# Kernel optimization log

Measured on AMD Instinct MI355X. Metric: run time of the kernel, lower is better.

Reference implementation:

```python
import jax, jax.numpy as jnp
import numpy as np

B, N, D = 2, 2048, 2048
H, HKV, HD = 16, 4, 128  # n_heads, n_kv_heads, head_dim
G = H // HKV             # GQA group size


def setup_inputs() -> dict:
    key = jax.random.key(0)
    ks = jax.random.split(key, 5)
    x = jax.random.normal(ks[0], (B, N, D), jnp.float32)
    # rotary angles: standard 10000-base frequencies, half head_dim
    inv_freq = 1.0 / (10000.0 ** (jnp.arange(HD // 2, dtype=jnp.float32) / (HD // 2)))
    ang = jnp.arange(N, dtype=jnp.float32)[:, None] * inv_freq[None, :]  # [N, HD/2]
    cos = jnp.cos(ang)[None, :, None, :]  # [1, N, 1, HD/2]
    sin = jnp.sin(ang)[None, :, None, :]
    attn_mask = jnp.ones((B, N), jnp.float32)
    s = 0.02
    Wq = jax.random.normal(ks[1], (D, H * HD), jnp.float32) * s
    Wkv = jax.random.normal(ks[2], (D, 2 * HKV * HD), jnp.float32) * s
    Wo = jax.random.normal(ks[3], (H * HD, D), jnp.float32) * s
    bo = jnp.zeros((D,), jnp.float32)
    return {"x": x, "cos": cos, "sin": sin, "attn_mask": attn_mask,
            "Wq": Wq, "Wkv": Wkv, "Wo": Wo, "bo": bo}


def _rope(t, cos, sin):
    # t: [b, n, h, d]; rotate-half style split at d//2
    d2 = t.shape[-1] // 2
    t1, t2 = t[..., :d2], t[..., d2:]
    return jnp.concatenate([t1 * cos + t2 * sin, t2 * cos - t1 * sin], axis=-1)


def reference(x, cos, sin, attn_mask, Wq, Wkv, Wo, bo):
    b, n, _ = x.shape
    q = (x @ Wq).reshape(b, n, H, HD)
    kv = x @ Wkv
    k, v = jnp.split(kv, 2, axis=-1)
    k = k.reshape(b, n, HKV, HD)
    v = v.reshape(b, n, HKV, HD)
    q = _rope(q, cos, sin)
    k = _rope(k, cos, sin)
    # b n h d -> b h n d; group q heads: head H_idx maps to kv head H_idx % HKV
    # (einops '(r h)' repeat pattern => q reshaped as [b, G, HKV, n, d])
    q = q.transpose(0, 2, 1, 3).reshape(b, G, HKV, n, HD)
    k = k.transpose(0, 2, 1, 3)  # [b, HKV, n, d]
    v = v.transpose(0, 2, 1, 3)
    scale = HD ** -0.5
    attn = jnp.einsum('bghnd,bhmd->bghnm', q, k) * scale
    bias = (1.0 - attn_mask) * -1e9  # [b, n_keys]
    attn = attn + bias[:, None, None, None, :]
    attn = jax.nn.softmax(attn, axis=-1)
    out = jnp.einsum('bghnm,bhmd->bghnd', attn, v)
    # b (g h) n d -> b n (g h d)
    out = out.transpose(0, 3, 1, 2, 4).reshape(b, n, H * HD)
    return out @ Wo + bo
```

## Files before the change

### kernel.cpp

```cpp
#include <hip/hip_runtime.h>
#include <hip/hip_bf16.h>
#include <cstddef>

#define NB    2
#define NSEQ  2048
#define DMODEL 2048
#define NH    16
#define NKV   4
#define HDIM  128

typedef __attribute__((ext_vector_type(8))) short short8;
typedef __attribute__((ext_vector_type(4))) short short4v;
typedef __attribute__((ext_vector_type(4))) float floatx4;
typedef const __attribute__((address_space(1))) void* gptr_t;
typedef __attribute__((address_space(3))) void* lptr_t;

#if __has_builtin(__builtin_amdgcn_exp2f)
#define EXP2F(x) __builtin_amdgcn_exp2f(x)
#else
#define EXP2F(x) __expf((x) * 0.6931471805599453f)
#endif

__device__ inline unsigned short f2bf(float f) {
    unsigned int u = __float_as_uint(f);
    u += 0x7fffu + ((u >> 16) & 1u);
    return (unsigned short)(u >> 16);
}

__device__ inline floatx4 fzero4() {
    floatx4 v; v[0] = 0.f; v[1] = 0.f; v[2] = 0.f; v[3] = 0.f; return v;
}

__global__ void cast_f32_bf16(const float* __restrict__ in,
                              unsigned short* __restrict__ out, int n4) {
    int i = blockIdx.x * blockDim.x + threadIdx.x;
    if (i >= n4) return;
    float4 v = ((const float4*)in)[i];
    ushort4 o;
    o.x = f2bf(v.x); o.y = f2bf(v.y); o.z = f2bf(v.z); o.w = f2bf(v.w);
    ((ushort4*)out)[i] = o;
}

__global__ void transpose_cast(const float* __restrict__ W,
                               unsigned short* __restrict__ Wt, int K, int N) {
    __shared__ float tile[32][33];
    int tx = threadIdx.x, ty = threadIdx.y;
    int n0 = blockIdx.x * 32, k0 = blockIdx.y * 32;
#pragma unroll
    for (int i = 0; i < 4; i++)
        tile[ty + i * 8][tx] = W[(size_t)(k0 + ty + i * 8) * N + n0 + tx];
    __syncthreads();
#pragma unroll
    for (int i = 0; i < 4; i++)
        Wt[(size_t)(n0 + ty + i * 8) * K + k0 + tx] = f2bf(tile[tx][ty + i * 8]);
}

__global__ __launch_bounds__(256, 2) void gemm_bt(
    const unsigned short* __restrict__ A,
    const unsigned short* __restrict__ Bt,
    float* __restrict__ C,
    const float* __restrict__ bias,
    int M, int N, int K) {
    __shared__ __align__(16) unsigned short As[128 * 32];
    __shared__ __align__(16) unsigned short Bs[128 * 32];
    const int t = threadIdx.x;
    const int m0 = blockIdx.y * 128, n0 = blockIdx.x * 128;
    const int lane = t & 63, wave = t >> 6;
    const int ln = lane & 15, quad = lane >> 4;
    const int wm = (wave >> 1) * 64, wn = (wave & 1) * 64;
    floatx4 acc[4][4];
#pragma unroll
    for (int r = 0; r < 4; r++)
#pragma unroll
        for (int c = 0; c < 4; c++) acc[r][c] = fzero4();

    const int r0 = t >> 2, c0 = (t & 3) * 8;
    const int r1 = (t + 256) >> 2, c1 = ((t + 256) & 3) * 8;

    for (int kt = 0; kt < K; kt += 32) {
        const unsigned short* ga0 = A + (size_t)(m0 + r0) * K + kt + c0;
        const unsigned short* ga1 = A + (size_t)(m0 + r1) * K + kt + c1;
        const unsigned short* gb0 = Bt + (size_t)(n0 + r0) * K + kt + c0;
        const unsigned short* gb1 = Bt + (size_t)(n0 + r1) * K + kt + c1;
        __builtin_amdgcn_global_load_lds((gptr_t)ga0, (lptr_t)(As + t * 8), 16, 0, 0);
        __builtin_amdgcn_global_load_lds((gptr_t)ga1, (lptr_t)(As + (t + 256) * 8), 16, 0, 0);
        __builtin_amdgcn_global_load_lds((gptr_t)gb0, (lptr_t)(Bs + t * 8), 16, 0, 0);
        __builtin_amdgcn_global_load_lds((gptr_t)gb1, (lptr_t)(Bs + (t + 256) * 8), 16, 0, 0);
        __syncthreads();
        short8 af[4], bfr[4];
#pragma unroll
        for (int r = 0; r < 4; r++)
            af[r] = *(const short8*)(As + (wm + r * 16 + ln) * 32 + quad * 8);
#pragma unroll
        for (int c = 0; c < 4; c++)
            bfr[c] = *(const short8*)(Bs + (wn + c * 16 + ln) * 32 + quad * 8);
#pragma unroll
        for (int r = 0; r < 4; r++)
#pragma unroll
            for (int c = 0; c < 4; c++)
                acc[r][c] = __builtin_amdgcn_mfma_f32_16x16x32_bf16(af[r], bfr[c], acc[r][c], 0, 0, 0);
        __syncthreads();
    }
#pragma unroll
    for (int r = 0; r < 4; r++) {
        int mb = m0 + wm + r * 16 + quad * 4;
#pragma unroll
        for (int c = 0; c < 4; c++) {
            int col = n0 + wn + c * 16 + ln;
            float bv = bias ? bias[col] : 0.f;
#pragma unroll
            for (int g = 0; g < 4; g++)
                C[(size_t)(mb + g) * N + col] = acc[r][c][g] + bv;
        }
    }
}

__global__ __launch_bounds__(256, 2) void gemm_qkv_rope(
    const unsigned short* __restrict__ A,
    const unsigned short* __restrict__ Bt,
    const float* __restrict__ cosb,
    const float* __restrict__ sinb,
    unsigned short* __restrict__ Qb,
    unsigned short* __restrict__ Kb,
    unsigned short* __restrict__ Vt) {
    const int K = DMODEL;
    __shared__ __align__(16) unsigned short As[128 * 32];
    __shared__ __align__(16) unsigned short Bs[128 * 32];
    __shared__ __align__(16) unsigned short Vx[128 * 136];
    const int t = threadIdx.x;
    const int m0 = blockIdx.y * 128, n0 = blockIdx.x * 128;
    const int lane = t & 63, wave = t >> 6;
    const int ln = lane & 15, quad = lane >> 4;
    const int wm = (wave >> 1) * 64, bq = (wave & 1) * 32;
    floatx4 acc[4][4];
#pragma unroll
    for (int r = 0; r < 4; r++)
#pragma unroll
        for (int c = 0; c < 4; c++) acc[r][c] = fzero4();

    const int r0 = t >> 2, c0 = (t & 3) * 8;
    const int r1 = (t + 256) >> 2, c1 = ((t + 256) & 3) * 8;

    for (int kt = 0; kt < K; kt += 32) {
        const unsigned short* ga0 = A + (size_t)(m0 + r0) * K + kt + c0;
        const unsigned short* ga1 = A + (size_t)(m0 + r1) * K + kt + c1;
        const unsigned short* gb0 = Bt + (size_t)(n0 + r0) * K + kt + c0;
        const unsigned short* gb1 = Bt + (size_t)(n0 + r1) * K + kt + c1;
        __builtin_amdgcn_global_load_lds((gptr_t)ga0, (lptr_t)(As + t * 8), 16, 0, 0);
        __builtin_amdgcn_global_load_lds((gptr_t)ga1, (lptr_t)(As + (t + 256) * 8), 16, 0, 0);
        __builtin_amdgcn_global_load_lds((gptr_t)gb0, (lptr_t)(Bs + t * 8), 16, 0, 0);
        __builtin_amdgcn_global_load_lds((gptr_t)gb1, (lptr_t)(Bs + (t + 256) * 8), 16, 0, 0);
        __syncthreads();
        short8 af[4], bfr[4];
#pragma unroll
        for (int r = 0; r < 4; r++)
            af[r] = *(const short8*)(As + (wm + r * 16 + ln) * 32 + quad * 8);
#pragma unroll
        for (int c = 0; c < 4; c++)
            bfr[c] = *(const short8*)(
                Bs + (bq + (c & 1) * 16 + (c >> 1) * 64 + ln) * 32 + quad * 8);
#pragma unroll
        for (int r = 0; r < 4; r++)
#pragma unroll
            for (int c = 0; c < 4; c++)
                acc[r][c] = __builtin_amdgcn_mfma_f32_16x16x32_bf16(af[r], bfr[c], acc[r][c], 0, 0, 0);
        __syncthreads();
    }

    if (n0 < 2048) {
        const float qs = (float)(0.08838834764831845 * 1.4426950408889634);
        int h = n0 >> 7;
#pragma unroll
        for (int r = 0; r < 4; r++)
#pragma unroll
            for (int c = 0; c < 2; c++)
#pragma unroll
                for (int g = 0; g < 4; g++) {
                    int row = m0 + wm + r * 16 + quad * 4 + g;
                    int b = row >> 11, n = row & 2047;
                    int j = bq + c * 16 + ln;
                    float cv = cosb[n * 64 + j], sv = sinb[n * 64 + j];
                    float t1 = acc[r][c][g], t2 = acc[r][c + 2][g];
                    unsigned short* qp = Qb + ((size_t)(b * NH + h) * NSEQ + n) * 128;
                    qp[j]      = f2bf((t1 * cv + t2 * sv) * qs);
                    qp[j + 64] = f2bf((t2 * cv - t1 * sv) * qs);
                }
    } else if (n0 < 2560) {
        int hk = (n0 - 2048) >> 7;
#pragma unroll
        for (int r = 0; r < 4; r++)
#pragma unroll
            for (int c = 0; c < 2; c++)
#pragma unroll
                for (int g = 0; g < 4; g++) {
                    int row = m0 + wm + r * 16 + quad * 4 + g;
                    int b = row >> 11, n = row & 2047;
                    int j = bq + c * 16 + ln;
                    float cv = cosb[n * 64 + j], sv = sinb[n * 64 + j];
                    float t1 = acc[r][c][g], t2 = acc[r][c + 2][g];
                    unsigned short* kp = Kb + ((size_t)(b * NKV + hk) * NSEQ + n) * 128;
                    kp[j]      = f2bf(t1 * cv + t2 * sv);
                    kp[j + 64] = f2bf(t2 * cv - t1 * sv);
                }
    } else {
        int hk = (n0 - 2560) >> 7;
#pragma unroll
        for (int r = 0; r < 4; r++)
#pragma unroll
            for (int c = 0; c < 4; c++) {
                int d = bq + (c & 1) * 16 + (c >> 1) * 64 + ln;
                int s = wm + (r >> 1) * 32 + quad * 8 + (r & 1) * 4;
#pragma unroll
                for (int g = 0; g < 4; g++)
                    Vx[d * 136 + s + g] = f2bf(acc[r][c][g]);
            }
        __syncthreads();
        int b = m0 >> 11, nloc = m0 & 2047;
#pragma unroll
        for (int pass = 0; pass < 2; pass++) {
            int d = pass * 64 + (t >> 2), q4 = t & 3;
            unsigned short* vp =
                Vt + ((size_t)(b * NKV + hk) * 128 + d) * NSEQ + nloc + q4 * 32;
#pragma unroll
            for (int i = 0; i < 4; i++)
                *(short8*)(vp + i * 8) = *(const short8*)(Vx + d * 136 + q4 * 32 + i * 8);
        }
    }
}

__global__ __launch_bounds__(256, 2) void attn_k(
    const unsigned short* __restrict__ Qb,
    const unsigned short* __restrict__ Kb,
    const unsigned short* __restrict__ Vt,
    const float* __restrict__ mask,
    unsigned short* __restrict__ Ab) {
    __shared__ __align__(16) unsigned short Ks[2 * 64 * 128];
    __shared__ __align__(16) unsigned short Vs[2 * 128 * 64];
    const int t = threadIdx.x, wave = t >> 6, lane = t & 63;
    const int ln = lane & 15, quad = lane >> 4;
    const int y = blockIdx.y, b = y >> 4, h = y & 15, kv = h & 3;
    const int q0 = blockIdx.x * 128;

    const unsigned short* Kbase = Kb + (size_t)(b * NKV + kv) * NSEQ * 128;
    const unsigned short* Vbase = Vt + (size_t)(b * NKV + kv) * 128 * NSEQ;
    const float* mbase = mask + b * NSEQ;

    const unsigned short* Qp =
        Qb + ((size_t)(b * NH + h) * NSEQ + q0 + wave * 32 + ln) * 128;
    short8 qf[2][4];
#pragma unroll
    for (int rt = 0; rt < 2; rt++)
#pragma unroll
        for (int kc = 0; kc < 4; kc++)
            qf[rt][kc] = *(const short8*)(Qp + rt * 16 * 128 + kc * 32 + quad * 8);

    floatx4 Oacc[2][8];
#pragma unroll
    for (int rt = 0; rt < 2; rt++)
#pragma unroll
        for (int d = 0; d < 8; d++) Oacc[rt][d] = fzero4();
    floatx4 Lacc[2];
    Lacc[0] = fzero4(); Lacc[1] = fzero4();

    short8 ones8;
#pragma unroll
    for (int i = 0; i < 8; i++) ones8[i] = (short)0x3F80;

    {
#pragma unroll
        for (int i = 0; i < 4; i++) {
            int c = i * 256 + t, r = c >> 4, c8 = c & 15;
            __builtin_amdgcn_global_load_lds(
                (gptr_t)(Kbase + (size_t)r * 128 + ((c8 ^ (r & 7)) * 8)),
                (lptr_t)(Ks + c * 8), 16, 0, 0);
        }
#pragma unroll
        for (int i = 0; i < 4; i++) {
            int c = i * 256 + t, dr = c >> 3, c8 = c & 7;
            __builtin_amdgcn_global_load_lds(
                (gptr_t)(Vbase + (size_t)dr * NSEQ + ((c8 ^ (dr & 7)) * 8)),
                (lptr_t)(Vs + c * 8), 16, 0, 0);
        }
    }
    __syncthreads();

    for (int it = 0; it < NSEQ / 64; ++it) {
        const int kt = it * 64, cb = it & 1;
        const int ktn = (kt + 64) & (NSEQ - 1);
        unsigned short* Kn = Ks + (cb ^ 1) * 8192;
        unsigned short* Vn = Vs + (cb ^ 1) * 8192;
#pragma unroll
        for (int i = 0; i < 4; i++) {
            int c = i * 256 + t, r = c >> 4, c8 = c & 15;
            __builtin_amdgcn_global_load_lds(
                (gptr_t)(Kbase + (size_t)(ktn + r) * 128 + ((c8 ^ (r & 7)) * 8)),
                (lptr_t)(Kn + c * 8), 16, 0, 0);
        }
#pragma unroll
        for (int i = 0; i < 4; i++) {
            int c = i * 256 + t, dr = c >> 3, c8 = c & 7;
            __builtin_amdgcn_global_load_lds(
                (gptr_t)(Vbase + (size_t)dr * NSEQ + ktn + ((c8 ^ (dr & 7)) * 8)),
                (lptr_t)(Vn + c * 8), 16, 0, 0);
        }

        floatx4 biasv[4];
#pragma unroll
        for (int nj = 0; nj < 4; nj++) {
            float4 mb = *(const float4*)(mbase + kt + nj * 16 + quad * 4);
            biasv[nj][0] = (1.f - mb.x) * -1.4426950408889634e9f;
            biasv[nj][1] = (1.f - mb.y) * -1.4426950408889634e9f;
            biasv[nj][2] = (1.f - mb.z) * -1.4426950408889634e9f;
            biasv[nj][3] = (1.f - mb.w) * -1.4426950408889634e9f;
        }

        const unsigned short* Kc = Ks + cb * 8192;
        const unsigned short* Vc = Vs + cb * 8192;

        floatx4 sacc[2][4];
#pragma unroll
        for (int rt = 0; rt < 2; rt++)
#pragma unroll
            for (int nj = 0; nj < 4; nj++) sacc[rt][nj] = fzero4();
#pragma unroll
        for (int kc = 0; kc < 4; kc++) {
            short8 kfv[4];
#pragma unroll
            for (int nj = 0; nj < 4; nj++)
                kfv[nj] = *(const short8*)(
                    Kc + (nj * 16 + ln) * 128 + (((kc * 4 + quad) ^ (ln & 7)) * 8));
#pragma unroll
            for (int rt = 0; rt < 2; rt++)
#pragma unroll
                for (int nj = 0; nj < 4; nj++)
                    sacc[rt][nj] = __builtin_amdgcn_mfma_f32_16x16x32_bf16(
                        kfv[nj], qf[rt][kc], sacc[rt][nj], 0, 0, 0);
        }

        short8 pf[2][2];
#pragma unroll
        for (int rt = 0; rt < 2; rt++)
#pragma unroll
            for (int p = 0; p < 2; p++)
#pragma unroll
                for (int e = 0; e < 2; e++) {
                    int nj = 2 * p + e;
#pragma unroll
                    for (int g = 0; g < 4; g++) {
                        float v = EXP2F(sacc[rt][nj][g] + biasv[nj][g]);
                        pf[rt][p][e * 4 + g] = (short)f2bf(v);
                    }
                }

#pragma unroll
        for (int rt = 0; rt < 2; rt++)
#pragma unroll
            for (int p = 0; p < 2; p++)
                Lacc[rt] = __builtin_amdgcn_mfma_f32_16x16x32_bf16(
                    ones8, pf[rt][p], Lacc[rt], 0, 0, 0);

#pragma unroll
        for (int dt = 0; dt < 8; dt++) {
            short8 vf[2];
#pragma unroll
            for (int p = 0; p < 2; p++)
                vf[p] = *(const short8*)(
                    Vc + (dt * 16 + ln) * 64 + (((p * 4 + quad) ^ (ln & 7)) * 8));
#pragma unroll
            for (int rt = 0; rt < 2; rt++) {
                floatx4 o = Oacc[rt][dt];
                o = __builtin_amdgcn_mfma_f32_16x16x32_bf16(vf[0], pf[rt][0], o, 0, 0, 0);
                o = __builtin_amdgcn_mfma_f32_16x16x32_bf16(vf[1], pf[rt][1], o, 0, 0, 0);
                Oacc[rt][dt] = o;
            }
        }
        __syncthreads();
    }

#pragma unroll
    for (int rt = 0; rt < 2; rt++) {
        float inv = 1.f / Lacc[rt][0];
        int row = q0 + wave * 32 + rt * 16 + ln;
        unsigned short* outp = Ab + (size_t)(b * NSEQ + row) * 2048 + h * 128;
#pragma unroll
        for (int dt = 0; dt < 8; dt++) {
            short4v o4;
#pragma unroll
            for (int g = 0; g < 4; g++) o4[g] = (short)f2bf(Oacc[rt][dt][g] * inv);
            *(short4v*)(outp + dt * 16 + quad * 4) = o4;
        }
    }
}

extern "C" void kernel_launch(void* const* d_in, const int* in_sizes, int n_in,
                              void* d_out, int out_size, void* d_ws, size_t ws_size,
                              hipStream_t stream) {
    const float* x    = (const float*)d_in[0];
    const float* cosb = (const float*)d_in[1];
    const float* sinb = (const float*)d_in[2];
    const float* mask = (const float*)d_in[3];
    const float* Wq   = (const float*)d_in[4];
    const float* Wkv  = (const float*)d_in[5];
    const float* Wo   = (const float*)d_in[6];
    const float* bo   = (const float*)d_in[7];
    float* out = (float*)d_out;

    char* ws = (char*)d_ws;
    unsigned short* xb  = (unsigned short*)ws; ws += (size_t)4096 * 2048 * 2;
    unsigned short* W1T = (unsigned short*)ws; ws += (size_t)3072 * 2048 * 2;
    unsigned short* WoT = (unsigned short*)ws; ws += (size_t)2048 * 2048 * 2;
    unsigned short* Qb  = (unsigned short*)ws; ws += (size_t)2 * 16 * 2048 * 128 * 2;
    unsigned short* Kb  = (unsigned short*)ws; ws += (size_t)2 * 4 * 2048 * 128 * 2;
    unsigned short* Vt  = (unsigned short*)ws; ws += (size_t)2 * 4 * 2048 * 128 * 2;
    unsigned short* Ab  = (unsigned short*)ws; ws += (size_t)2 * 2048 * 2048 * 2;

    cast_f32_bf16<<<8192, 256, 0, stream>>>(x, xb, 2097152);
    dim3 tb(32, 8);
    transpose_cast<<<dim3(64, 64), tb, 0, stream>>>(Wq, W1T, 2048, 2048);
    transpose_cast<<<dim3(32, 64), tb, 0, stream>>>(Wkv, W1T + (size_t)2048 * 2048, 2048, 1024);
    transpose_cast<<<dim3(64, 64), tb, 0, stream>>>(Wo, WoT, 2048, 2048);
    gemm_qkv_rope<<<dim3(24, 32), 256, 0, stream>>>(xb, W1T, cosb, sinb, Qb, Kb, Vt);
    attn_k<<<dim3(16, 32), 256, 0, stream>>>(Qb, Kb, Vt, mask, Ab);
    gemm_bt<<<dim3(16, 32), 256, 0, stream>>>(Ab, WoT, out, bo, 4096, 2048, 2048);
}
```

Measured before the change: 320.4 us.

## Fuse prep kernels, precompute mask bias, and streamline attention inner loop

Merges the x cast, three weight transpose-casts and a new mask-to-bias precompute into one prep kernel launch, cutting launch overhead. The attention kernel now reads a precomputed bias, hoists the swizzled LDS addresses out of the loop, unrolls the double-buffer loop by two so buffer offsets are compile-time constants, and packs P to bf16 by truncation with a byte permute instead of round-to-nearest. Truncation slightly changes rounding of the softmax numerator.

```diff
diff --git a/kernel.cpp b/kernel.cpp
--- a/kernel.cpp
+++ b/kernel.cpp
@@ -27,25 +27,49 @@
     return (unsigned short)(u >> 16);
 }
 
+__device__ inline unsigned int pk2bf_trunc(float a, float b) {
+    return __builtin_amdgcn_perm(__float_as_uint(b), __float_as_uint(a), 0x07060302u);
+}
+
 __device__ inline floatx4 fzero4() {
     floatx4 v; v[0] = 0.f; v[1] = 0.f; v[2] = 0.f; v[3] = 0.f; return v;
 }
 
-__global__ void cast_f32_bf16(const float* __restrict__ in,
-                              unsigned short* __restrict__ out, int n4) {
-    int i = blockIdx.x * blockDim.x + threadIdx.x;
-    if (i >= n4) return;
-    float4 v = ((const float4*)in)[i];
-    ushort4 o;
-    o.x = f2bf(v.x); o.y = f2bf(v.y); o.z = f2bf(v.z); o.w = f2bf(v.w);
-    ((ushort4*)out)[i] = o;
-}
-
-__global__ void transpose_cast(const float* __restrict__ W,
-                               unsigned short* __restrict__ Wt, int K, int N) {
+__global__ void prep_k(const float* __restrict__ x, const float* __restrict__ Wq,
+                       const float* __restrict__ Wkv, const float* __restrict__ Wo,
+                       const float* __restrict__ mask,
+                       unsigned short* __restrict__ xb,
+                       unsigned short* __restrict__ W1T,
+                       unsigned short* __restrict__ WoT,
+                       float* __restrict__ bias2) {
     __shared__ float tile[32][33];
-    int tx = threadIdx.x, ty = threadIdx.y;
-    int n0 = blockIdx.x * 32, k0 = blockIdx.y * 32;
+    const int bid = blockIdx.x, t = threadIdx.x;
+    if (bid < 8192) {
+        int i = bid * 256 + t;
+        float4 v = ((const float4*)x)[i];
+        ushort4 o;
+        o.x = f2bf(v.x); o.y = f2bf(v.y); o.z = f2bf(v.z); o.w = f2bf(v.w);
+        ((ushort4*)xb)[i] = o;
+        return;
+    }
+    if (bid >= 18432) {
+        int i = (bid - 18432) * 1024 + t * 4;
+        float4 m = *(const float4*)(mask + i);
+        const float c = -1.4426950408889634e9f;
+        float4 o;
+        o.x = (1.f - m.x) * c; o.y = (1.f - m.y) * c;
+        o.z = (1.f - m.z) * c; o.w = (1.f - m.w) * c;
+        *(float4*)(bias2 + i) = o;
+        return;
+    }
+    const float* W; unsigned short* Wt; int N, local;
+    if (bid < 12288)      { W = Wq;  Wt = W1T;                       N = 2048; local = bid - 8192; }
+    else if (bid < 14336) { W = Wkv; Wt = W1T + (size_t)2048 * 2048; N = 1024; local = bid - 12288; }
+    else                  { W = Wo;  Wt = WoT;                       N = 2048; local = bid - 14336; }
+    const int K = 2048;
+    int nt = N >> 5;
+    int bx = local % nt, by = local / nt;
+    int n0 = bx * 32, k0 = by * 32, tx = t & 31, ty = t >> 5;
 #pragma unroll
     for (int i = 0; i < 4; i++)
         tile[ty + i * 8][tx] = W[(size_t)(k0 + ty + i * 8) * N + n0 + tx];
@@ -232,7 +256,7 @@
     const unsigned short* __restrict__ Qb,
     const unsigned short* __restrict__ Kb,
     const unsigned short* __restrict__ Vt,
-    const float* __restrict__ mask,
+    const float* __restrict__ bias2,
     unsigned short* __restrict__ Ab) {
     __shared__ __align__(16) unsigned short Ks[2 * 64 * 128];
     __shared__ __align__(16) unsigned short Vs[2 * 128 * 64];
@@ -243,7 +267,7 @@
 
     const unsigned short* Kbase = Kb + (size_t)(b * NKV + kv) * NSEQ * 128;
     const unsigned short* Vbase = Vt + (size_t)(b * NKV + kv) * 128 * NSEQ;
-    const float* mbase = mask + b * NSEQ;
+    const float* bbase = bias2 + b * NSEQ;
 
     const unsigned short* Qp =
         Qb + ((size_t)(b * NH + h) * NSEQ + q0 + wave * 32 + ln) * 128;
@@ -254,6 +278,15 @@
         for (int kc = 0; kc < 4; kc++)
             qf[rt][kc] = *(const short8*)(Qp + rt * 16 * 128 + kc * 32 + quad * 8);
 
+    const char* kp[4];
+#pragma unroll
+    for (int kc = 0; kc < 4; kc++)
+        kp[kc] = (const char*)Ks + ln * 256 + (((kc * 4 + quad) ^ (ln & 7)) * 16);
+    const char* vp[2];
+#pragma unroll
+    for (int p = 0; p < 2; p++)
+        vp[p] = (const char*)Vs + ln * 128 + (((p * 4 + quad) ^ (ln & 7)) * 16);
+
     floatx4 Oacc[2][8];
 #pragma unroll
     for (int rt = 0; rt < 2; rt++)
@@ -266,115 +299,100 @@
 #pragma unroll
     for (int i = 0; i < 8; i++) ones8[i] = (short)0x3F80;
 
-    {
-#pragma unroll
-        for (int i = 0; i < 4; i++) {
-            int c = i * 256 + t, r = c >> 4, c8 = c & 15;
-            __builtin_amdgcn_global_load_lds(
-                (gptr_t)(Kbase + (size_t)r * 128 + ((c8 ^ (r & 7)) * 8)),
-                (lptr_t)(Ks + c * 8), 16, 0, 0);
-        }
-#pragma unroll
-        for (int i = 0; i < 4; i++) {
-            int c = i * 256 + t, dr = c >> 3, c8 = c & 7;
-            __builtin_amdgcn_global_load_lds(
-                (gptr_t)(Vbase + (size_t)dr * NSEQ + ((c8 ^ (dr & 7)) * 8)),
-                (lptr_t)(Vs + c * 8), 16, 0, 0);
-        }
-    }
-    __syncthreads();
-
-    for (int it = 0; it < NSEQ / 64; ++it) {
-        const int kt = it * 64, cb = it & 1;
-        const int ktn = (kt + 64) & (NSEQ - 1);
-        unsigned short* Kn = Ks + (cb ^ 1) * 8192;
-        unsigned short* Vn = Vs + (cb ^ 1) * 8192;
+    auto stage = [&](int ktn, int buf) {
 #pragma unroll
         for (int i = 0; i < 4; i++) {
             int c = i * 256 + t, r = c >> 4, c8 = c & 15;
             __builtin_amdgcn_global_load_lds(
                 (gptr_t)(Kbase + (size_t)(ktn + r) * 128 + ((c8 ^ (r & 7)) * 8)),
-                (lptr_t)(Kn + c * 8), 16, 0, 0);
+                (lptr_t)(Ks + buf * 8192 + c * 8), 16, 0, 0);
         }
 #pragma unroll
         for (int i = 0; i < 4; i++) {
             int c = i * 256 + t, dr = c >> 3, c8 = c & 7;
             __builtin_amdgcn_global_load_lds(
                 (gptr_t)(Vbase + (size_t)dr * NSEQ + ktn + ((c8 ^ (dr & 7)) * 8)),
-                (lptr_t)(Vn + c * 8), 16, 0, 0);
-        }
-
-        floatx4 biasv[4];
-#pragma unroll
-        for (int nj = 0; nj < 4; nj++) {
-            float4 mb = *(const float4*)(mbase + kt + nj * 16 + quad * 4);
-            biasv[nj][0] = (1.f - mb.x) * -1.4426950408889634e9f;
-            biasv[nj][1] = (1.f - mb.y) * -1.4426950408889634e9f;
-            biasv[nj][2] = (1.f - mb.z) * -1.4426950408889634e9f;
-            biasv[nj][3] = (1.f - mb.w) * -1.4426950408889634e9f;
-        }
-
-        const unsigned short* Kc = Ks + cb * 8192;
-        const unsigned short* Vc = Vs + cb * 8192;
-
-        floatx4 sacc[2][4];
-#pragma unroll
-        for (int rt = 0; rt < 2; rt++)
-#pragma unroll
-            for (int nj = 0; nj < 4; nj++) sacc[rt][nj] = fzero4();
-#pragma unroll
-        for (int kc = 0; kc < 4; kc++) {
-            short8 kfv[4];
+                (lptr_t)(Vs + buf * 8192 + c * 8), 16, 0, 0);
+        }
+    };
+
+    stage(0, 0);
+    __syncthreads();
+
+#pragma unroll 1
+    for (int it2 = 0; it2 < NSEQ / 128; ++it2) {
+#pragma unroll
+        for (int half = 0; half < 2; ++half) {
+            const int it = it2 * 2 + half;
+            const int kt = it * 64;
+            const int ktn = (kt + 64) & (NSEQ - 1);
+            stage(ktn, half ^ 1);
+            const int off = half * 16384;
+
+            floatx4 biasv[4];
 #pragma unroll
             for (int nj = 0; nj < 4; nj++)
-                kfv[nj] = *(const short8*)(
-                    Kc + (nj * 16 + ln) * 128 + (((kc * 4 + quad) ^ (ln & 7)) * 8));
+                biasv[nj] = *(const floatx4*)(bbase + kt + nj * 16 + quad * 4);
+
+            floatx4 sacc[2][4];
 #pragma unroll
             for (int rt = 0; rt < 2; rt++)
 #pragma unroll
+                for (int nj = 0; nj < 4; nj++) sacc[rt][nj] = fzero4();
+#pragma unroll
+            for (int kc = 0; kc < 4; kc++) {
+                short8 kfv[4];
+#pragma unroll
                 for (int nj = 0; nj < 4; nj++)
-                    sacc[rt][nj] = __builtin_amdgcn_mfma_f32_16x16x32_bf16(
-                        kfv[nj], qf[rt][kc], sacc[rt][nj], 0, 0, 0);
-        }
-
-        short8 pf[2][2];
-#pragma unroll
-        for (int rt = 0; rt < 2; rt++)
-#pragma unroll
-            for (int p = 0; p < 2; p++)
-#pragma unroll
-                for (int e = 0; e < 2; e++) {
-                    int nj = 2 * p + e;
-#pragma unroll
-                    for (int g = 0; g < 4; g++) {
-                        float v = EXP2F(sacc[rt][nj][g] + biasv[nj][g]);
-                        pf[rt][p][e * 4 + g] = (short)f2bf(v);
+                    kfv[nj] = *(const short8*)(kp[kc] + off + nj * 4096);
+#pragma unroll
+                for (int rt = 0; rt < 2; rt++)
+#pragma unroll
+                    for (int nj = 0; nj < 4; nj++)
+                        sacc[rt][nj] = __builtin_amdgcn_mfma_f32_16x16x32_bf16(
+                            kfv[nj], qf[rt][kc], sacc[rt][nj], 0, 0, 0);
+            }
+
+            short8 pf[2][2];
+#pragma unroll
+            for (int rt = 0; rt < 2; rt++)
+#pragma unroll
+                for (int p = 0; p < 2; p++) {
+                    union { short8 s; unsigned int w[4]; } pu;
+#pragma unroll
+                    for (int e = 0; e < 2; e++) {
+                        int nj = 2 * p + e;
+                        float e0 = EXP2F(sacc[rt][nj][0] + biasv[nj][0]);
+                        float e1 = EXP2F(sacc[rt][nj][1] + biasv[nj][1]);
+                        float e2 = EXP2F(sacc[rt][nj][2] + biasv[nj][2]);
+                        float e3 = EXP2F(sacc[rt][nj][3] + biasv[nj][3]);
+                        pu.w[e * 2 + 0] = pk2bf_trunc(e0, e1);
+                        pu.w[e * 2 + 1] = pk2bf_trunc(e2, e3);
                     }
+                    pf[rt][p] = pu.s;
                 }
 
 #pragma unroll
-        for (int rt = 0; rt < 2; rt++)
-#pragma unroll
-            for (int p = 0; p < 2; p++)
-                Lacc[rt] = __builtin_amdgcn_mfma_f32_16x16x32_bf16(
-                    ones8, pf[rt][p], Lacc[rt], 0, 0, 0);
-
-#pragma unroll
-        for (int dt = 0; dt < 8; dt++) {
-            short8 vf[2];
-#pragma unroll
-            for (int p = 0; p < 2; p++)
-                vf[p] = *(const short8*)(
-                    Vc + (dt * 16 + ln) * 64 + (((p * 4 + quad) ^ (ln & 7)) * 8));
-#pragma unroll
-            for (int rt = 0; rt < 2; rt++) {
-                floatx4 o = Oacc[rt][dt];
-                o = __builtin_amdgcn_mfma_f32_16x16x32_bf16(vf[0], pf[rt][0], o, 0, 0, 0);
-                o = __builtin_amdgcn_mfma_f32_16x16x32_bf16(vf[1], pf[rt][1], o, 0, 0, 0);
-                Oacc[rt][dt] = o;
+            for (int rt = 0; rt < 2; rt++)
+#pragma unroll
+                for (int p = 0; p < 2; p++)
+                    Lacc[rt] = __builtin_amdgcn_mfma_f32_16x16x32_bf16(
+                        ones8, pf[rt][p], Lacc[rt], 0, 0, 0);
+
+#pragma unroll
+            for (int dt = 0; dt < 8; dt++) {
+                short8 vf0 = *(const short8*)(vp[0] + off + dt * 2048);
+                short8 vf1 = *(const short8*)(vp[1] + off + dt * 2048);
+#pragma unroll
+                for (int rt = 0; rt < 2; rt++) {
+                    floatx4 o = Oacc[rt][dt];
+                    o = __builtin_amdgcn_mfma_f32_16x16x32_bf16(vf0, pf[rt][0], o, 0, 0, 0);
+                    o = __builtin_amdgcn_mfma_f32_16x16x32_bf16(vf1, pf[rt][1], o, 0, 0, 0);
+                    Oacc[rt][dt] = o;
+                }
             }
-        }
-        __syncthreads();
+            __syncthreads();
+        }
     }
 
 #pragma unroll
@@ -413,13 +431,10 @@
     unsigned short* Kb  = (unsigned short*)ws; ws += (size_t)2 * 4 * 2048 * 128 * 2;
     unsigned short* Vt  = (unsigned short*)ws; ws += (size_t)2 * 4 * 2048 * 128 * 2;
     unsigned short* Ab  = (unsigned short*)ws; ws += (size_t)2 * 2048 * 2048 * 2;
-
-    cast_f32_bf16<<<8192, 256, 0, stream>>>(x, xb, 2097152);
-    dim3 tb(32, 8);
-    transpose_cast<<<dim3(64, 64), tb, 0, stream>>>(Wq, W1T, 2048, 2048);
-    transpose_cast<<<dim3(32, 64), tb, 0, stream>>>(Wkv, W1T + (size_t)2048 * 2048, 2048, 1024);
-    transpose_cast<<<dim3(64, 64), tb, 0, stream>>>(Wo, WoT, 2048, 2048);
+    float* bias2 = (float*)ws;                 ws += (size_t)NB * NSEQ * 4;
+
+    prep_k<<<18436, 256, 0, stream>>>(x, Wq, Wkv, Wo, mask, xb, W1T, WoT, bias2);
     gemm_qkv_rope<<<dim3(24, 32), 256, 0, stream>>>(xb, W1T, cosb, sinb, Qb, Kb, Vt);
-    attn_k<<<dim3(16, 32), 256, 0, stream>>>(Qb, Kb, Vt, mask, Ab);
+    attn_k<<<dim3(16, 32), 256, 0, stream>>>(Qb, Kb, Vt, bias2, Ab);
     gemm_bt<<<dim3(16, 32), 256, 0, stream>>>(Ab, WoT, out, bo, 4096, 2048, 2048);
 }
```

After: 312.3 us. -2.5%, faster.
